# Kernel optimization log

Hardware: AMD Instinct MI355X
Metric: run time of the kernel (lower is better)

The kernel has to match this reference:

```python
import jax, jax.numpy as jnp
import numpy as np

HIDDEN = 1024
HEADS = 16
HEAD_DIM = HIDDEN // HEADS
B, S = 2, 2048


def setup_inputs() -> dict:
    key = jax.random.key(0)
    ks = jax.random.split(key, 11)
    std = 1.0 / np.sqrt(HIDDEN)
    return {
        "query": jax.random.normal(ks[0], (B, S, HIDDEN), dtype=jnp.float32),
        "key": jax.random.normal(ks[1], (B, S, HIDDEN), dtype=jnp.float32),
        "value": jax.random.normal(ks[2], (B, S, HIDDEN), dtype=jnp.float32),
        "Wq": jax.random.uniform(ks[3], (HIDDEN, HIDDEN), jnp.float32, -std, std),
        "bq": jax.random.uniform(ks[4], (HIDDEN,), jnp.float32, -std, std),
        "Wk": jax.random.uniform(ks[5], (HIDDEN, HIDDEN), jnp.float32, -std, std),
        "bk": jax.random.uniform(ks[6], (HIDDEN,), jnp.float32, -std, std),
        "Wv": jax.random.uniform(ks[7], (HIDDEN, HIDDEN), jnp.float32, -std, std),
        "bv": jax.random.uniform(ks[8], (HIDDEN,), jnp.float32, -std, std),
        "Wo": jax.random.uniform(ks[9], (HIDDEN, HIDDEN), jnp.float32, -std, std),
        "bo": jax.random.uniform(ks[10], (HIDDEN,), jnp.float32, -std, std),
    }


def reference(query, key, value, Wq, bq, Wk, bk, Wv, bv, Wo, bo):
    b = query.shape[0]
    scale = jnp.sqrt(jnp.float32(HEAD_DIM))
    # linear projections (torch Linear: x @ W.T + b), split into heads -> [b, h, s, d]
    def proj(x, W, bias):
        y = x @ W.T + bias
        return y.reshape(b, -1, HEADS, HEAD_DIM).transpose(0, 2, 1, 3)
    Q = proj(query, Wq, bq)
    K = proj(key, Wk, bk)
    V = proj(value, Wv, bv)
    scores = jnp.einsum("bhqd,bhkd->bhqk", Q, K) / scale
    attn = jax.nn.softmax(scores, axis=-1)
    ctx = jnp.einsum("bhqk,bhkd->bhqd", attn, V)
    ctx = ctx.transpose(0, 2, 1, 3).reshape(b, -1, HIDDEN)
    return ctx @ Wo.T + bo
```

## Files before the change

kernel.cpp:

```cpp
#include <hip/hip_runtime.h>

typedef __attribute__((ext_vector_type(8))) short short8;
typedef __attribute__((ext_vector_type(2))) float float2_t;
typedef __attribute__((ext_vector_type(4))) float float4_t;
typedef __attribute__((ext_vector_type(16))) float f32x16;
typedef __attribute__((ext_vector_type(4))) unsigned int uint4_t;
typedef __attribute__((ext_vector_type(2))) unsigned int uint2_t;
typedef unsigned short u16;

#define HIDDEN 1024
#define HDIM   64
#define SS     2048
#define TOK    4096
#define QSCALE 0.1803368801111137f

__device__ __forceinline__ unsigned int fbits(float f) {
  unsigned int x; __builtin_memcpy(&x, &f, 4); return x;
}
__device__ __forceinline__ u16 f2bf(float f) {
  return (u16)((fbits(f) + 0x8000u) >> 16);
}
__device__ __forceinline__ unsigned int pk2bf(float a, float b) {
  return __builtin_amdgcn_perm(fbits(b) + 0x8000u, fbits(a) + 0x8000u, 0x07060302);
}
__device__ __forceinline__ unsigned int pk2bf_t(float a, float b) {
  return __builtin_amdgcn_perm(fbits(b), fbits(a), 0x07060302);
}

__device__ __forceinline__ void gl_lds16(const u16* g, u16* l) {
  __builtin_amdgcn_global_load_lds(
      (const __attribute__((address_space(1))) unsigned int*)g,
      (__attribute__((address_space(3))) unsigned int*)l, 16, 0, 0);
}

__global__ __launch_bounds__(256) void convert_all(
    const float* __restrict__ w0, const float* __restrict__ w1,
    const float* __restrict__ w2, const float* __restrict__ w3,
    const float* __restrict__ x0, const float* __restrict__ x1,
    const float* __restrict__ x2, u16* __restrict__ Wall, u16* __restrict__ Xall) {
  int y = blockIdx.y;
  const float* src; u16* dst;
  if (y < 4) {
    if (blockIdx.x >= 512) return;
    src = y == 0 ? w0 : y == 1 ? w1 : y == 2 ? w2 : w3;
    dst = Wall + ((size_t)y << 20);
  } else {
    src = y == 4 ? x0 : y == 5 ? x1 : x2;
    dst = Xall + ((size_t)(y - 4) << 22);
  }
  int g = (blockIdx.x * 256 + threadIdx.x) * 8;
  float4_t a = *(const float4_t*)(src + g);
  float4_t b = *(const float4_t*)(src + g + 4);
  uint4_t o;
  o.x = pk2bf(a[0], a[1]); o.y = pk2bf(a[2], a[3]);
  o.z = pk2bf(b[0], b[1]); o.w = pk2bf(b[2], b[3]);
  *(uint4_t*)(dst + g) = o;
}

template<int MTILES, bool AXF32, bool OUTF32>
__device__ __forceinline__ void gemm_bt_body(
    const void* __restrict__ X, const u16* __restrict__ Wb,
    const float* __restrict__ bias, void* __restrict__ Y, int mode, float oscale,
    u16* sA, u16* sB, int row0, int col0) {
  const int tid  = threadIdx.x;
  const int wv   = tid >> 6, lane = tid & 63, quad = lane >> 4, ln = lane & 15;
  const int wm   = (wv >> 1) * (MTILES * 16), wn = (wv & 1) * 64;
  constexpr int AITERS = MTILES;

  float4_t acc[MTILES][4];
#pragma unroll
  for (int i = 0; i < MTILES; i++)
#pragma unroll
    for (int j = 0; j < 4; j++) acc[i][j] = (float4_t)0.0f;

  for (int kt = 0; kt < 16; ++kt) {
    const int k0 = kt * 64;
    short8 ax[AITERS];
    if (AXF32) {
#pragma unroll
      for (int i = 0; i < AITERS; i++) {
        int idx = i * 256 + tid, r = idx >> 3, c = idx & 7;
        const float* p = (const float*)X + (size_t)(row0 + r) * HIDDEN + k0 + c * 8;
        float4_t a = *(const float4_t*)p;
        float4_t b = *(const float4_t*)(p + 4);
        union { unsigned int u[4]; short8 s; } x;
        x.u[0] = pk2bf(a[0], a[1]); x.u[1] = pk2bf(a[2], a[3]);
        x.u[2] = pk2bf(b[0], b[1]); x.u[3] = pk2bf(b[2], b[3]);
        ax[i] = x.s;
      }
    }
    __syncthreads();
#pragma unroll
    for (int i = 0; i < 4; i++) {
      int idx = i * 256 + tid, r = idx >> 3, c = idx & 7;
      int gc = c ^ (r & 7);
      gl_lds16(Wb + (size_t)(col0 + r) * HIDDEN + k0 + gc * 8, sB + idx * 8);
    }
    if (AXF32) {
#pragma unroll
      for (int i = 0; i < AITERS; i++) {
        int idx = i * 256 + tid, r = idx >> 3, c = idx & 7;
        int pos = c ^ (r & 7);
        *(short8*)(sA + r * 64 + pos * 8) = ax[i];
      }
    } else {
#pragma unroll
      for (int i = 0; i < AITERS; i++) {
        int idx = i * 256 + tid, r = idx >> 3, c = idx & 7;
        int gc = c ^ (r & 7);
        gl_lds16((const u16*)X + (size_t)(row0 + r) * HIDDEN + k0 + gc * 8, sA + idx * 8);
      }
    }
    __syncthreads();

    short8 af[MTILES][2], bfr[4][2];
#pragma unroll
    for (int mt = 0; mt < MTILES; mt++)
#pragma unroll
      for (int kk = 0; kk < 2; kk++) {
        int r = wm + mt * 16 + ln;
        int ch = kk * 4 + quad;
        af[mt][kk] = *(const short8*)(sA + r * 64 + (ch ^ (r & 7)) * 8);
      }
#pragma unroll
    for (int nt = 0; nt < 4; nt++)
#pragma unroll
      for (int kk = 0; kk < 2; kk++) {
        int r = wn + nt * 16 + ln;
        int ch = kk * 4 + quad;
        bfr[nt][kk] = *(const short8*)(sB + r * 64 + (ch ^ (r & 7)) * 8);
      }
#pragma unroll
    for (int kk = 0; kk < 2; kk++)
#pragma unroll
      for (int mt = 0; mt < MTILES; mt++)
#pragma unroll
        for (int nt = 0; nt < 4; nt++)
          acc[mt][nt] = __builtin_amdgcn_mfma_f32_16x16x32_bf16(af[mt][kk], bfr[nt][kk], acc[mt][nt], 0, 0, 0);
  }

  float bcol[4];
#pragma unroll
  for (int nt = 0; nt < 4; nt++) bcol[nt] = bias[col0 + wn + nt * 16 + ln];
#pragma unroll
  for (int mt = 0; mt < MTILES; mt++)
#pragma unroll
    for (int nt = 0; nt < 4; nt++) {
      int n = col0 + wn + nt * 16 + ln;
#pragma unroll
      for (int r = 0; r < 4; r++) {
        int m = row0 + wm + mt * 16 + quad * 4 + r;
        float v = (acc[mt][nt][r] + bcol[nt]) * oscale;
        if (mode == 0) {
          if (OUTF32) ((float*)Y)[(size_t)m * HIDDEN + n] = v;
          else        ((u16*)Y)[(size_t)m * HIDDEN + n] = f2bf(v);
        } else {
          ((u16*)Y)[((size_t)(m >> 11) * HIDDEN + n) * SS + (m & 2047)] = f2bf(v);
        }
      }
    }
}

__global__ __launch_bounds__(256) void qkv_gemm_bf16(
    const u16* __restrict__ Xall, const u16* __restrict__ Wall,
    const float* __restrict__ bq, const float* __restrict__ bk, const float* __restrict__ bv,
    u16* __restrict__ Qp, u16* __restrict__ Kp, u16* __restrict__ Vt) {
  __shared__ u16 sA[128 * 64];
  __shared__ u16 sB[128 * 64];
  int z = blockIdx.z;
  const u16* X = Xall + ((size_t)z << 22);
  const u16* W = Wall + ((size_t)z << 20);
  const float* Bp = z == 0 ? bq : z == 1 ? bk : bv;
  u16* Y = z == 0 ? Qp : z == 1 ? Kp : Vt;
  int mode = (z == 2) ? 1 : 0;
  float sc = (z == 0) ? QSCALE : 1.0f;
  gemm_bt_body<4, false, false>(X, W, Bp, Y, mode, sc, sA, sB, blockIdx.y * 128, blockIdx.x * 128);
}

__global__ __launch_bounds__(256) void qkv_gemm_f32(
    const float* __restrict__ xq, const float* __restrict__ xk, const float* __restrict__ xv,
    const u16* __restrict__ Wall,
    const float* __restrict__ bq, const float* __restrict__ bk, const float* __restrict__ bv,
    u16* __restrict__ Qp, u16* __restrict__ Kp, u16* __restrict__ Vt) {
  __shared__ u16 sA[128 * 64];
  __shared__ u16 sB[128 * 64];
  int z = blockIdx.z;
  const float* X = z == 0 ? xq : z == 1 ? xk : xv;
  const u16* W = Wall + ((size_t)z << 20);
  const float* Bp = z == 0 ? bq : z == 1 ? bk : bv;
  u16* Y = z == 0 ? Qp : z == 1 ? Kp : Vt;
  int mode = (z == 2) ? 1 : 0;
  float sc = (z == 0) ? QSCALE : 1.0f;
  gemm_bt_body<4, true, false>(X, W, Bp, Y, mode, sc, sA, sB, blockIdx.y * 128, blockIdx.x * 128);
}

__global__ __launch_bounds__(256) void out_gemm(
    const u16* __restrict__ X, const u16* __restrict__ Wob,
    const float* __restrict__ bias, float* __restrict__ Y) {
  __shared__ u16 sA[64 * 64];
  __shared__ u16 sB[128 * 64];
  gemm_bt_body<2, false, true>(X, Wob, bias, Y, 0, 1.0f, sA, sB, blockIdx.y * 64, blockIdx.x * 128);
}

__global__ __launch_bounds__(256, 2) void attn(
    const u16* __restrict__ Qp, const u16* __restrict__ Kp,
    const u16* __restrict__ Vt, u16* __restrict__ Ctx) {
  __shared__ u16 sK[2][128 * 64];
  __shared__ u16 sV[2][64 * 128];
  const int tid  = threadIdx.x;
  const int wv   = tid >> 6, lane = tid & 63;
  const int l5   = lane >> 5, ln = lane & 31;
  const int f = blockIdx.x;
  const int qt = f >> 5, g = f & 31, h = g >> 1, b = g & 1;
  const int row0w = qt * 128 + wv * 32;

  short8 qf[4];
#pragma unroll
  for (int kk = 0; kk < 4; ++kk)
    qf[kk] = *(const short8*)(Qp + (size_t)(b * SS + row0w + ln) * HIDDEN
                              + h * HDIM + kk * 16 + l5 * 8);

  f32x16 oacc[2];
  oacc[0] = (f32x16)0.0f; oacc[1] = (f32x16)0.0f;
  float dsum = 0.f;

  auto stage = [&](int buf, int kt) {
#pragma unroll
    for (int p = 0; p < 4; ++p) {
      int off = p * 256 + tid;
      { int r = off >> 3, c = off & 7;  int gc = c ^ (r & 7);
        gl_lds16(Kp + (size_t)(b * SS + kt * 128 + r) * HIDDEN + h * HDIM + gc * 8,
                 &sK[buf][0] + off * 8); }
      { int r = off >> 4, c = off & 15; int gc = c ^ (r & 15);
        gl_lds16(Vt + ((size_t)b * HIDDEN + h * HDIM + r) * SS + kt * 128 + gc * 8,
                 &sV[buf][0] + off * 8); }
    }
  };

  stage(0, 0);
  __syncthreads();

#pragma unroll 2
  for (int kt = 0; kt < 16; ++kt) {
    const int cur = kt & 1;
    if (kt < 15) stage(cur ^ 1, kt + 1);
    const u16* K_ = &sK[cur][0];
    const u16* V_ = &sV[cur][0];

    f32x16 st[4];
    __builtin_amdgcn_s_setprio(1);
#pragma unroll
    for (int kgg = 0; kgg < 4; ++kgg) {
      st[kgg] = (f32x16)0.0f;
#pragma unroll
      for (int kk = 0; kk < 4; ++kk) {
        int r = kgg * 32 + ln;
        int ch = kk * 2 + l5;
        short8 kf = *(const short8*)(K_ + r * 64 + ((ch ^ (r & 7))) * 8);
        st[kgg] = __builtin_amdgcn_mfma_f32_32x32x16_bf16(kf, qf[kk], st[kgg], 0, 0, 0);
      }
    }
    __builtin_amdgcn_s_setprio(0);

#pragma unroll
    for (int kgg = 0; kgg < 4; ++kgg) {
      union PF { unsigned int u[4]; short8 s; };
      PF pfr[2];
      {
        float p[16];
#pragma unroll
        for (int r = 0; r < 16; ++r)
          p[r] = __builtin_amdgcn_exp2f(fminf(st[kgg][r], 80.f));
        float2_t t0 = (float2_t){p[0], p[1]}   + (float2_t){p[2], p[3]};
        float2_t t1 = (float2_t){p[4], p[5]}   + (float2_t){p[6], p[7]};
        float2_t t2 = (float2_t){p[8], p[9]}   + (float2_t){p[10], p[11]};
        float2_t t3 = (float2_t){p[12], p[13]} + (float2_t){p[14], p[15]};
        float2_t t4 = (t0 + t1) + (t2 + t3);
        dsum += t4.x + t4.y;
        unsigned int pk[8];
#pragma unroll
        for (int i = 0; i < 8; ++i) pk[i] = pk2bf_t(p[2 * i], p[2 * i + 1]);
        uint2_t r02 = __builtin_amdgcn_permlane32_swap(pk[0], pk[2], false, false);
        uint2_t r13 = __builtin_amdgcn_permlane32_swap(pk[1], pk[3], false, false);
        uint2_t r46 = __builtin_amdgcn_permlane32_swap(pk[4], pk[6], false, false);
        uint2_t r57 = __builtin_amdgcn_permlane32_swap(pk[5], pk[7], false, false);
        pfr[0].u[0] = r02.x; pfr[0].u[1] = r13.x;
        pfr[0].u[2] = r02.y; pfr[0].u[3] = r13.y;
        pfr[1].u[0] = r46.x; pfr[1].u[1] = r57.x;
        pfr[1].u[2] = r46.y; pfr[1].u[3] = r57.y;
      }

      __builtin_amdgcn_s_setprio(1);
#pragma unroll
      for (int ks = 0; ks < 2; ++ks) {
        int ch = (kgg * 2 + ks) * 2 + l5;
#pragma unroll
        for (int dg = 0; dg < 2; ++dg) {
          int r = dg * 32 + ln;
          short8 vf = *(const short8*)(V_ + r * 128 + ((ch ^ (r & 15))) * 8);
          oacc[dg] = __builtin_amdgcn_mfma_f32_32x32x16_bf16(vf, pfr[ks].s, oacc[dg], 0, 0, 0);
        }
      }
      __builtin_amdgcn_s_setprio(0);
    }
    __syncthreads();
  }

  float s = dsum + __shfl_xor(dsum, 32, 64);
  float inv = 1.0f / s;

  u16* ep = ((u16*)sK) + wv * 2048;
  {
    int row = ln;
#pragma unroll
    for (int dg = 0; dg < 2; ++dg)
#pragma unroll
      for (int i = 0; i < 4; ++i) {
        uint2_t w;
        w.x = pk2bf(oacc[dg][4 * i] * inv,     oacc[dg][4 * i + 1] * inv);
        w.y = pk2bf(oacc[dg][4 * i + 2] * inv, oacc[dg][4 * i + 3] * inv);
        int c = dg * 4 + i;
        *(uint2_t*)(ep + row * 64 + ((c ^ (row & 7))) * 8 + l5 * 4) = w;
      }
  }
#pragma unroll
  for (int ps = 0; ps < 4; ++ps) {
    int r = ps * 8 + (lane >> 3);
    int c = lane & 7;
    short8 o8 = *(const short8*)(ep + r * 64 + ((c ^ (r & 7))) * 8);
    *(short8*)(Ctx + (size_t)(b * SS + row0w + r) * HIDDEN + h * HDIM + c * 8) = o8;
  }
}

extern "C" void kernel_launch(void* const* d_in, const int* in_sizes, int n_in,
                              void* d_out, int out_size, void* d_ws, size_t ws_size,
                              hipStream_t stream) {
  const float* q  = (const float*)d_in[0];
  const float* k  = (const float*)d_in[1];
  const float* v  = (const float*)d_in[2];
  const float* Wq = (const float*)d_in[3];
  const float* bq = (const float*)d_in[4];
  const float* Wk = (const float*)d_in[5];
  const float* bk = (const float*)d_in[6];
  const float* Wv = (const float*)d_in[7];
  const float* bv = (const float*)d_in[8];
  const float* Wo = (const float*)d_in[9];
  const float* bo = (const float*)d_in[10];

  u16* Qp   = (u16*)d_ws;
  u16* Kp   = Qp + (size_t)TOK * HIDDEN;
  u16* Vt   = Kp + (size_t)TOK * HIDDEN;
  u16* Wall = Vt + (size_t)TOK * HIDDEN;
  u16* Xall = Wall + (4u << 20);
  u16* Cx   = Qp;
  bool useX = ws_size >= (size_t)56 * 1024 * 1024;

  dim3 blk(256);
  if (useX) {
    hipLaunchKernelGGL(convert_all, dim3(2048, 7), blk, 0, stream,
                       Wq, Wk, Wv, Wo, q, k, v, Wall, Xall);
    hipLaunchKernelGGL(qkv_gemm_bf16, dim3(8, 32, 3), blk, 0, stream,
                       Xall, Wall, bq, bk, bv, Qp, Kp, Vt);
  } else {
    hipLaunchKernelGGL(convert_all, dim3(512, 4), blk, 0, stream,
                       Wq, Wk, Wv, Wo, q, k, v, Wall, Wall);
    hipLaunchKernelGGL(qkv_gemm_f32, dim3(8, 32, 3), blk, 0, stream,
                       q, k, v, Wall, bq, bk, bv, Qp, Kp, Vt);
  }
  hipLaunchKernelGGL(attn, dim3(512), blk, 0, stream, Qp, Kp, Vt, Cx);
  hipLaunchKernelGGL(out_gemm, dim3(8, 64, 1), blk, 0, stream,
                     Cx, Wall + (3u << 20), bo, (float*)d_out);
}
```

Measured before the change: 221.5 us.

## Double-buffer GEMM LDS tiles, swizzle block order, drop separate input conversion pass

Rewrites the shared GEMM body to double-buffer the A and B tiles in LDS. The next k-tile's global loads are issued before the current tile's MFMAs, and the loop needs one barrier per iteration instead of two. Blocks are remapped into groups of 8 row tiles for better L2 reuse of the weights. The path that first converted the activations to a bf16 buffer is removed, so the QKV GEMM always reads the fp32 activations and converts them in registers. This saves a separate conversion pass but doubles LDS use, which may lower occupancy.

```diff
diff --git a/kernel.cpp b/kernel.cpp
--- a/kernel.cpp
+++ b/kernel.cpp
@@ -58,14 +58,15 @@
 }
 
 template<int MTILES, bool AXF32, bool OUTF32>
-__device__ __forceinline__ void gemm_bt_body(
+__device__ __forceinline__ void gemm_dbuf(
     const void* __restrict__ X, const u16* __restrict__ Wb,
     const float* __restrict__ bias, void* __restrict__ Y, int mode, float oscale,
     u16* sA, u16* sB, int row0, int col0) {
   const int tid  = threadIdx.x;
   const int wv   = tid >> 6, lane = tid & 63, quad = lane >> 4, ln = lane & 15;
   const int wm   = (wv >> 1) * (MTILES * 16), wn = (wv & 1) * 64;
-  constexpr int AITERS = MTILES;
+  constexpr int ASZ = MTILES * 32 * 64;
+  constexpr int BSZ = 128 * 64;
 
   float4_t acc[MTILES][4];
 #pragma unroll
@@ -73,45 +74,69 @@
 #pragma unroll
     for (int j = 0; j < 4; j++) acc[i][j] = (float4_t)0.0f;
 
-  for (int kt = 0; kt < 16; ++kt) {
+  auto stageB = [&](int buf, int kt) {
     const int k0 = kt * 64;
-    short8 ax[AITERS];
-    if (AXF32) {
-#pragma unroll
-      for (int i = 0; i < AITERS; i++) {
-        int idx = i * 256 + tid, r = idx >> 3, c = idx & 7;
-        const float* p = (const float*)X + (size_t)(row0 + r) * HIDDEN + k0 + c * 8;
-        float4_t a = *(const float4_t*)p;
-        float4_t b = *(const float4_t*)(p + 4);
-        union { unsigned int u[4]; short8 s; } x;
-        x.u[0] = pk2bf(a[0], a[1]); x.u[1] = pk2bf(a[2], a[3]);
-        x.u[2] = pk2bf(b[0], b[1]); x.u[3] = pk2bf(b[2], b[3]);
-        ax[i] = x.s;
-      }
-    }
-    __syncthreads();
 #pragma unroll
     for (int i = 0; i < 4; i++) {
       int idx = i * 256 + tid, r = idx >> 3, c = idx & 7;
       int gc = c ^ (r & 7);
-      gl_lds16(Wb + (size_t)(col0 + r) * HIDDEN + k0 + gc * 8, sB + idx * 8);
-    }
-    if (AXF32) {
-#pragma unroll
-      for (int i = 0; i < AITERS; i++) {
-        int idx = i * 256 + tid, r = idx >> 3, c = idx & 7;
-        int pos = c ^ (r & 7);
-        *(short8*)(sA + r * 64 + pos * 8) = ax[i];
-      }
-    } else {
-#pragma unroll
-      for (int i = 0; i < AITERS; i++) {
-        int idx = i * 256 + tid, r = idx >> 3, c = idx & 7;
-        int gc = c ^ (r & 7);
-        gl_lds16((const u16*)X + (size_t)(row0 + r) * HIDDEN + k0 + gc * 8, sA + idx * 8);
-      }
-    }
-    __syncthreads();
+      gl_lds16(Wb + (size_t)(col0 + r) * HIDDEN + k0 + gc * 8, sB + buf * BSZ + idx * 8);
+    }
+  };
+  auto stageA_bf16 = [&](int buf, int kt) {
+    const int k0 = kt * 64;
+#pragma unroll
+    for (int i = 0; i < MTILES; i++) {
+      int idx = i * 256 + tid, r = idx >> 3, c = idx & 7;
+      int gc = c ^ (r & 7);
+      gl_lds16((const u16*)X + (size_t)(row0 + r) * HIDDEN + k0 + gc * 8,
+               sA + buf * ASZ + idx * 8);
+    }
+  };
+  auto loadA_f32 = [&](int kt, float4_t (&ax)[MTILES][2]) {
+    const int k0 = kt * 64;
+#pragma unroll
+    for (int i = 0; i < MTILES; i++) {
+      int idx = i * 256 + tid, r = idx >> 3, c = idx & 7;
+      const float* p = (const float*)X + (size_t)(row0 + r) * HIDDEN + k0 + c * 8;
+      ax[i][0] = *(const float4_t*)p;
+      ax[i][1] = *(const float4_t*)(p + 4);
+    }
+  };
+  auto writeA_f32 = [&](int buf, float4_t (&ax)[MTILES][2]) {
+#pragma unroll
+    for (int i = 0; i < MTILES; i++) {
+      int idx = i * 256 + tid, r = idx >> 3, c = idx & 7;
+      int pos = c ^ (r & 7);
+      union { unsigned int u[4]; short8 s; } x;
+      x.u[0] = pk2bf(ax[i][0][0], ax[i][0][1]); x.u[1] = pk2bf(ax[i][0][2], ax[i][0][3]);
+      x.u[2] = pk2bf(ax[i][1][0], ax[i][1][1]); x.u[3] = pk2bf(ax[i][1][2], ax[i][1][3]);
+      *(short8*)(sA + buf * ASZ + r * 64 + pos * 8) = x.s;
+    }
+  };
+
+  if (AXF32) {
+    float4_t ax0[MTILES][2];
+    loadA_f32(0, ax0);
+    stageB(0, 0);
+    writeA_f32(0, ax0);
+  } else {
+    stageB(0, 0);
+    stageA_bf16(0, 0);
+  }
+  __syncthreads();
+
+#pragma unroll 2
+  for (int kt = 0; kt < 16; ++kt) {
+    const int cur = kt & 1;
+    float4_t axn[MTILES][2];
+    if (AXF32) { if (kt < 15) loadA_f32(kt + 1, axn); }
+    if (kt < 15) {
+      stageB(cur ^ 1, kt + 1);
+      if (!AXF32) stageA_bf16(cur ^ 1, kt + 1);
+    }
+    const u16* A_ = sA + cur * ASZ;
+    const u16* B_ = sB + cur * BSZ;
 
     short8 af[MTILES][2], bfr[4][2];
 #pragma unroll
@@ -120,7 +145,7 @@
       for (int kk = 0; kk < 2; kk++) {
         int r = wm + mt * 16 + ln;
         int ch = kk * 4 + quad;
-        af[mt][kk] = *(const short8*)(sA + r * 64 + (ch ^ (r & 7)) * 8);
+        af[mt][kk] = *(const short8*)(A_ + r * 64 + (ch ^ (r & 7)) * 8);
       }
 #pragma unroll
     for (int nt = 0; nt < 4; nt++)
@@ -128,7 +153,7 @@
       for (int kk = 0; kk < 2; kk++) {
         int r = wn + nt * 16 + ln;
         int ch = kk * 4 + quad;
-        bfr[nt][kk] = *(const short8*)(sB + r * 64 + (ch ^ (r & 7)) * 8);
+        bfr[nt][kk] = *(const short8*)(B_ + r * 64 + (ch ^ (r & 7)) * 8);
       }
 #pragma unroll
     for (int kk = 0; kk < 2; kk++)
@@ -137,6 +162,9 @@
 #pragma unroll
         for (int nt = 0; nt < 4; nt++)
           acc[mt][nt] = __builtin_amdgcn_mfma_f32_16x16x32_bf16(af[mt][kk], bfr[nt][kk], acc[mt][nt], 0, 0, 0);
+
+    if (AXF32) { if (kt < 15) writeA_f32(cur ^ 1, axn); }
+    __syncthreads();
   }
 
   float bcol[4];
@@ -161,45 +189,33 @@
     }
 }
 
-__global__ __launch_bounds__(256) void qkv_gemm_bf16(
-    const u16* __restrict__ Xall, const u16* __restrict__ Wall,
-    const float* __restrict__ bq, const float* __restrict__ bk, const float* __restrict__ bv,
-    u16* __restrict__ Qp, u16* __restrict__ Kp, u16* __restrict__ Vt) {
-  __shared__ u16 sA[128 * 64];
-  __shared__ u16 sB[128 * 64];
-  int z = blockIdx.z;
-  const u16* X = Xall + ((size_t)z << 22);
-  const u16* W = Wall + ((size_t)z << 20);
-  const float* Bp = z == 0 ? bq : z == 1 ? bk : bv;
-  u16* Y = z == 0 ? Qp : z == 1 ? Kp : Vt;
-  int mode = (z == 2) ? 1 : 0;
-  float sc = (z == 0) ? QSCALE : 1.0f;
-  gemm_bt_body<4, false, false>(X, W, Bp, Y, mode, sc, sA, sB, blockIdx.y * 128, blockIdx.x * 128);
-}
-
-__global__ __launch_bounds__(256) void qkv_gemm_f32(
+__global__ __launch_bounds__(256) void qkv_gemm(
     const float* __restrict__ xq, const float* __restrict__ xk, const float* __restrict__ xv,
     const u16* __restrict__ Wall,
     const float* __restrict__ bq, const float* __restrict__ bk, const float* __restrict__ bv,
     u16* __restrict__ Qp, u16* __restrict__ Kp, u16* __restrict__ Vt) {
-  __shared__ u16 sA[128 * 64];
-  __shared__ u16 sB[128 * 64];
+  __shared__ u16 sA[2 * 128 * 64];
+  __shared__ u16 sB[2 * 128 * 64];
   int z = blockIdx.z;
+  int fid = blockIdx.x, g = fid & 7, j = fid >> 3;
+  int xb = j & 7, yb = g + 8 * (j >> 3);
   const float* X = z == 0 ? xq : z == 1 ? xk : xv;
   const u16* W = Wall + ((size_t)z << 20);
   const float* Bp = z == 0 ? bq : z == 1 ? bk : bv;
   u16* Y = z == 0 ? Qp : z == 1 ? Kp : Vt;
   int mode = (z == 2) ? 1 : 0;
   float sc = (z == 0) ? QSCALE : 1.0f;
-  gemm_bt_body<4, true, false>(X, W, Bp, Y, mode, sc, sA, sB, blockIdx.y * 128, blockIdx.x * 128);
+  gemm_dbuf<4, true, false>(X, W, Bp, Y, mode, sc, sA, sB, yb * 128, xb * 128);
 }
 
 __global__ __launch_bounds__(256) void out_gemm(
     const u16* __restrict__ X, const u16* __restrict__ Wob,
     const float* __restrict__ bias, float* __restrict__ Y) {
-  __shared__ u16 sA[64 * 64];
-  __shared__ u16 sB[128 * 64];
-  gemm_bt_body<2, false, true>(X, Wob, bias, Y, 0, 1.0f, sA, sB, blockIdx.y * 64, blockIdx.x * 128);
+  __shared__ u16 sA[2 * 64 * 64];
+  __shared__ u16 sB[2 * 128 * 64];
+  int fid = blockIdx.x, g = fid & 7, j = fid >> 3;
+  int xb = j & 7, yb = g + 8 * (j >> 3);
+  gemm_dbuf<2, false, true>(X, Wob, bias, Y, 0, 1.0f, sA, sB, yb * 64, xb * 128);
 }
 
 __global__ __launch_bounds__(256, 2) void attn(
@@ -351,23 +367,14 @@
   u16* Kp   = Qp + (size_t)TOK * HIDDEN;
   u16* Vt   = Kp + (size_t)TOK * HIDDEN;
   u16* Wall = Vt + (size_t)TOK * HIDDEN;
-  u16* Xall = Wall + (4u << 20);
   u16* Cx   = Qp;
-  bool useX = ws_size >= (size_t)56 * 1024 * 1024;
 
   dim3 blk(256);
-  if (useX) {
-    hipLaunchKernelGGL(convert_all, dim3(2048, 7), blk, 0, stream,
-                       Wq, Wk, Wv, Wo, q, k, v, Wall, Xall);
-    hipLaunchKernelGGL(qkv_gemm_bf16, dim3(8, 32, 3), blk, 0, stream,
-                       Xall, Wall, bq, bk, bv, Qp, Kp, Vt);
-  } else {
-    hipLaunchKernelGGL(convert_all, dim3(512, 4), blk, 0, stream,
-                       Wq, Wk, Wv, Wo, q, k, v, Wall, Wall);
-    hipLaunchKernelGGL(qkv_gemm_f32, dim3(8, 32, 3), blk, 0, stream,
-                       q, k, v, Wall, bq, bk, bv, Qp, Kp, Vt);
-  }
+  hipLaunchKernelGGL(convert_all, dim3(512, 4), blk, 0, stream,
+                     Wq, Wk, Wv, Wo, q, k, v, Wall, Wall);
+  hipLaunchKernelGGL(qkv_gemm, dim3(256, 1, 3), blk, 0, stream,
+                     q, k, v, Wall, bq, bk, bv, Qp, Kp, Vt);
   hipLaunchKernelGGL(attn, dim3(512), blk, 0, stream, Qp, Kp, Vt, Cx);
-  hipLaunchKernelGGL(out_gemm, dim3(8, 64, 1), blk, 0, stream,
+  hipLaunchKernelGGL(out_gemm, dim3(512), blk, 0, stream,
                      Cx, Wall + (3u << 20), bo, (float*)d_out);
 }
```

After: 232.6 us. 1.05x slower.
